# Kernel tuning notes

Hardware: AMD Instinct MI355X
Metric: run time of the kernel (lower is better)

## Reference

```python
import jax, jax.numpy as jnp
import numpy as np
from jax import lax

B = 4096
PRO_VOCAB, PRO_LEN, PRO_K = 25, 1000, 8
LIG_VOCAB, LIG_LEN, LIG_K = 64, 100, 4
CH = 96  # 2*CH = 192 = 6*32 per the reshape in the original forward
DN = ('NCH', 'OIH', 'NCH')  # 1D conv dimension numbers


def setup_inputs() -> dict:
    key = jax.random.key(0)
    ks = jax.random.split(key, 8)
    protein = jax.random.normal(ks[0], (B, PRO_VOCAB, PRO_LEN), dtype=jnp.float32)
    ligand = jax.random.normal(ks[1], (B, LIG_VOCAB, LIG_LEN), dtype=jnp.float32)
    w_pro = jax.random.normal(ks[2], (CH, PRO_VOCAB, PRO_K), dtype=jnp.float32) * 0.05
    b_pro = jnp.zeros((CH,), dtype=jnp.float32)
    w_lig = jax.random.normal(ks[3], (CH, LIG_VOCAB, LIG_K), dtype=jnp.float32) * 0.05
    b_lig = jnp.zeros((CH,), dtype=jnp.float32)
    # QuLinear readout over the 32*32=1024 amplitude-encoded Gram matrix -> scalar
    w_aff = jax.random.normal(ks[4], (1024,), dtype=jnp.float32) * 0.05
    b_aff = jnp.zeros((), dtype=jnp.float32)
    return {"protein": protein, "ligand": ligand, "w_pro": w_pro, "b_pro": b_pro,
            "w_lig": w_lig, "b_lig": b_lig, "w_aff": w_aff, "b_aff": b_aff}


def _conv_branch(x, w, b):
    # Conv1d (valid) -> ReLU -> global max pool over length  =>  (B, CH)
    y = lax.conv_general_dilated(x, w, (1,), 'VALID', dimension_numbers=DN)
    return jnp.max(jax.nn.relu(y + b[None, :, None]), axis=-1)


def reference(protein, ligand, w_pro, b_pro, w_lig, b_lig, w_aff, b_aff):
    x1 = _conv_branch(ligand, w_lig, b_lig)    # (B, 96)
    x2 = _conv_branch(protein, w_pro, b_pro)   # (B, 96)
    x = jnp.concatenate([x1, x2], axis=1).reshape(-1, 6, 32)  # (B, 6, 32)
    # Vectorized per-sample Gram matrix a.T @ a : (B, 32, 32)
    gram = jnp.einsum('bij,bik->bjk', x, x)
    flat = gram.reshape(gram.shape[0], -1)     # (B, 1024)
    # Amplitude encoding: L2-normalize the flattened Gram matrix per sample
    amp = flat / (jnp.linalg.norm(flat, axis=1, keepdims=True) + 1e-12)
    # QuLinear readout -> scalar affinity per sample
    aff = amp @ w_aff + b_aff                  # (B,)
    return aff
```

## Files before the change

### kernel.cpp

```cpp
#include <hip/hip_runtime.h>
#include <math.h>

typedef _Float16 f16;
typedef _Float16 f16x2 __attribute__((ext_vector_type(2)));
typedef _Float16 f16x4 __attribute__((ext_vector_type(4)));
typedef _Float16 f16x8 __attribute__((ext_vector_type(8)));
typedef float f32x4 __attribute__((ext_vector_type(4)));

__global__ void repack_pro_kernel(const float* __restrict__ w, f16* __restrict__ wp) {
    constexpr int V = 25, K = 8;
    int i = blockIdx.x * 256 + threadIdx.x;
    if (i >= K * 6 * 64 * 8) return;
    int e = i & 7, l = (i >> 3) & 63, c6 = (i >> 9) % 6, t = i / (512 * 6);
    int r16 = l & 15, g = l >> 4;
    int ch = c6 * 16 + r16, v = g * 8 + e;
    float val = (v < V) ? w[(ch * V + v) * K + t] : 0.f;
    wp[i] = (f16)val;
}

__global__ void repack_lig_kernel(const float* __restrict__ w, f16* __restrict__ wp) {
    constexpr int V = 64, K = 4;
    int i = blockIdx.x * 256 + threadIdx.x;
    if (i >= 8 * 6 * 64 * 8) return;
    int e = i & 7, l = (i >> 3) & 63, c6 = (i >> 9) % 6, tk = i / (512 * 6);
    int t = tk >> 1, ks = tk & 1;
    int r16 = l & 15, g = l >> 4;
    int ch = c6 * 16 + r16, v = ks * 32 + g * 8 + e;
    wp[i] = (f16)w[(ch * V + v) * K + t];
}

__global__ __launch_bounds__(512, 4) void conv_kernel(
    const float* __restrict__ pro,
    const f16*   __restrict__ wpP,
    const float* __restrict__ bP,
    const float* __restrict__ lig,
    const f16*   __restrict__ wpL,
    const float* __restrict__ bL,
    float* __restrict__ feat,
    int B)
{
    __shared__ __align__(16) char s_raw[264 * 80];
    __shared__ __align__(16) f16  s_w[24576];
    __shared__ float s_red[8 * 96];

    const int tid  = threadIdx.x;
    const int wave = tid >> 6;
    const int lane = tid & 63;
    const int g    = lane >> 4;
    const int r16  = lane & 15;

    if ((int)blockIdx.x < B) {
        constexpr int V = 25, L = 1000, KT = 8, LOUT = 993;
        constexpr int CH = 256, NC = 4, BR = 264, RSB = 80;
        constexpr int P4 = BR / 4;
        constexpr int NU = 7 * P4;
        const size_t b = blockIdx.x;
        const float* gs = pro + b * (size_t)(V * L);
        const int rw = wave & 3, cw = wave >> 2;

        {   const f16x8* wg = (const f16x8*)wpP;
            f16x8* wl = (f16x8*)s_w;
            #pragma unroll
            for (int u = 0; u < 24576 / 8 / 512; ++u)
                wl[u * 512 + tid] = wg[u * 512 + tid];
        }
        for (int row = tid; row < BR; row += 512) {
            const int swz = ((row >> 3) & 3) << 4;
            *(f16x8*)(s_raw + row * RSB + (48 ^ swz)) = (f16x8){};
        }
        __syncthreads();

        float runmax[3];
        #pragma unroll
        for (int c3 = 0; c3 < 3; ++c3) runmax[c3] = -3.0e38f;

        for (int c = 0; c < NC; ++c) {
            if (c) __syncthreads();
            if (tid < NU) {
                const int vq = tid / P4, p4 = tid - vq * P4;
                const int p = 4 * p4, gp = c * CH + p;
                float4 x0 = {0.f,0.f,0.f,0.f}, x1 = {0.f,0.f,0.f,0.f};
                float4 x2 = {0.f,0.f,0.f,0.f}, x3 = {0.f,0.f,0.f,0.f};
                if (gp < L) {
                    x0 = *(const float4*)(gs + (size_t)(4 * vq) * L + gp);
                    if (vq < 6) {
                        x1 = *(const float4*)(gs + (size_t)(4 * vq + 1) * L + gp);
                        x2 = *(const float4*)(gs + (size_t)(4 * vq + 2) * L + gp);
                        x3 = *(const float4*)(gs + (size_t)(4 * vq + 3) * L + gp);
                    }
                }
                const int pb = 8 * vq;
                const int slot = pb & 48, sub = pb & 8;
                const float a0[4] = {x0.x, x0.y, x0.z, x0.w};
                const float a1[4] = {x1.x, x1.y, x1.z, x1.w};
                const float a2[4] = {x2.x, x2.y, x2.z, x2.w};
                const float a3[4] = {x3.x, x3.y, x3.z, x3.w};
                #pragma unroll
                for (int j = 0; j < 4; ++j) {
                    const int row = p + j;
                    const int swz = ((row >> 3) & 3) << 4;
                    f16x4 hv = { (f16)a0[j], (f16)a1[j], (f16)a2[j], (f16)a3[j] };
                    *(f16x4*)(s_raw + row * RSB + ((slot ^ swz) + sub)) = hv;
                }
            }
            __syncthreads();

            f32x4 acc[4][3] = {};
            #pragma unroll 1
            for (int t = 0; t < KT; ++t) {
                f16x8 bf[3];
                #pragma unroll
                for (int c3 = 0; c3 < 3; ++c3)
                    bf[c3] = *(const f16x8*)(s_w + ((t * 6 + cw * 3 + c3) * 64 + lane) * 8);
                #pragma unroll
                for (int rt = 0; rt < 4; ++rt) {
                    const int row = rw * 64 + rt * 16 + r16 + t;
                    const int swz = ((row >> 3) & 3) << 4;
                    f16x8 a = *(const f16x8*)(s_raw + row * RSB + ((g * 16) ^ swz));
                    #pragma unroll
                    for (int c3 = 0; c3 < 3; ++c3)
                        acc[rt][c3] = __builtin_amdgcn_mfma_f32_16x16x32_f16(a, bf[c3], acc[rt][c3], 0, 0, 0);
                }
            }
            #pragma unroll
            for (int rt = 0; rt < 4; ++rt) {
                const int pt = c * CH + rw * 64 + rt * 16;
                if (pt + 16 <= LOUT) {
                    #pragma unroll
                    for (int c3 = 0; c3 < 3; ++c3)
                        #pragma unroll
                        for (int i = 0; i < 4; ++i)
                            runmax[c3] = fmaxf(runmax[c3], acc[rt][c3][i]);
                } else {
                    const int p0g = pt + g * 4;
                    #pragma unroll
                    for (int c3 = 0; c3 < 3; ++c3)
                        #pragma unroll
                        for (int i = 0; i < 4; ++i)
                            if (p0g + i < LOUT) runmax[c3] = fmaxf(runmax[c3], acc[rt][c3][i]);
                }
            }
        }

        #pragma unroll
        for (int c3 = 0; c3 < 3; ++c3) {
            runmax[c3] = fmaxf(runmax[c3], __shfl_xor(runmax[c3], 16, 64));
            runmax[c3] = fmaxf(runmax[c3], __shfl_xor(runmax[c3], 32, 64));
        }
        if (lane < 16) {
            #pragma unroll
            for (int c3 = 0; c3 < 3; ++c3)
                s_red[wave * 48 + c3 * 16 + lane] = runmax[c3];
        }
        __syncthreads();
        if (tid < 96) {
            const int cw2 = tid / 48, chs = tid - cw2 * 48;
            float m = s_red[(cw2 * 4) * 48 + chs];
            #pragma unroll
            for (int rw2 = 1; rw2 < 4; ++rw2)
                m = fmaxf(m, s_red[(cw2 * 4 + rw2) * 48 + chs]);
            feat[b * 192 + 96 + tid] = fmaxf(m + bP[tid], 0.f);
        }
    } else {
        constexpr int V = 64, L = 100, KT = 4, LOUT = 97;
        constexpr int BR = 120, RSB = 144;
        constexpr int P4 = BR / 4, NU = 32 * P4;
        const size_t b = blockIdx.x - B;
        const float* gs = lig + b * (size_t)(V * L);

        {   const f16x8* wg = (const f16x8*)wpL;
            f16x8* wl = (f16x8*)s_w;
            #pragma unroll
            for (int u = 0; u < 24576 / 8 / 512; ++u)
                wl[u * 512 + tid] = wg[u * 512 + tid];
        }
        #pragma unroll
        for (int u = 0; u < 2; ++u) {
            const int i = u * 512 + tid;
            if (i < NU) {
                const int v2 = i / P4, p4 = i - v2 * P4;
                const int p  = 4 * p4;
                float4 x0 = {0.f, 0.f, 0.f, 0.f}, x1 = {0.f, 0.f, 0.f, 0.f};
                if (p < L) {
                    x0 = *(const float4*)(gs + (size_t)(2 * v2) * L + p);
                    x1 = *(const float4*)(gs + (size_t)(2 * v2 + 1) * L + p);
                }
                const int pb = 4 * v2;
                const int slot = pb & 0x70, sub = pb & 12;
                const float vx0[4] = {x0.x, x0.y, x0.z, x0.w};
                const float vx1[4] = {x1.x, x1.y, x1.z, x1.w};
                #pragma unroll
                for (int j = 0; j < 4; ++j) {
                    const int row = p + j;
                    const int swz = ((row >> 3) & 3) << 4;
                    f16x2 hv = { (f16)vx0[j], (f16)vx1[j] };
                    *(f16x2*)(s_raw + row * RSB + ((slot ^ swz) + sub)) = hv;
                }
            }
        }
        __syncthreads();

        if (wave < 7) {
            f32x4 acc[6] = {};
            #pragma unroll 1
            for (int t = 0; t < KT; ++t) {
                #pragma unroll
                for (int ks = 0; ks < 2; ++ks) {
                    f16x8 bf[6];
                    #pragma unroll
                    for (int c6 = 0; c6 < 6; ++c6)
                        bf[c6] = *(const f16x8*)(s_w + (((t * 2 + ks) * 6 + c6) * 64 + lane) * 8);
                    const int row = wave * 16 + r16 + t;
                    const int swz = ((row >> 3) & 3) << 4;
                    f16x8 a = *(const f16x8*)(s_raw + row * RSB + ((ks * 64 + g * 16) ^ swz));
                    #pragma unroll
                    for (int c6 = 0; c6 < 6; ++c6)
                        acc[c6] = __builtin_amdgcn_mfma_f32_16x16x32_f16(a, bf[c6], acc[c6], 0, 0, 0);
                }
            }
            float runmax[6];
            const int p0g = wave * 16 + g * 4;
            #pragma unroll
            for (int c6 = 0; c6 < 6; ++c6) {
                runmax[c6] = -3.0e38f;
                #pragma unroll
                for (int i = 0; i < 4; ++i)
                    if (p0g + i < LOUT) runmax[c6] = fmaxf(runmax[c6], acc[c6][i]);
                runmax[c6] = fmaxf(runmax[c6], __shfl_xor(runmax[c6], 16, 64));
                runmax[c6] = fmaxf(runmax[c6], __shfl_xor(runmax[c6], 32, 64));
            }
            if (lane < 16) {
                #pragma unroll
                for (int c6 = 0; c6 < 6; ++c6)
                    s_red[wave * 96 + c6 * 16 + lane] = runmax[c6];
            }
        }
        __syncthreads();
        if (tid < 96) {
            float m = s_red[tid];
            #pragma unroll
            for (int w = 1; w < 7; ++w) m = fmaxf(m, s_red[w * 96 + tid]);
            feat[b * 192 + tid] = fmaxf(m + bL[tid], 0.f);
        }
    }
}

__global__ __launch_bounds__(256) void gram_affinity_kernel(
    const float* __restrict__ feat, const float* __restrict__ w_aff,
    const float* __restrict__ b_aff, float* __restrict__ out, int B)
{
    const int lane = threadIdx.x & 63;
    const int wid  = threadIdx.x >> 6;
    const int b    = blockIdx.x * 4 + wid;

    __shared__ float s_x[4][192];

    if (b < B) {
        const float* fp = feat + (size_t)b * 192;
        for (int i = lane; i < 192; i += 64) s_x[wid][i] = fp[i];
    }
    __syncthreads();

    if (b < B) {
        float ssum = 0.f, sdot = 0.f;
        #pragma unroll
        for (int t = 0; t < 16; ++t) {
            const int jk = t * 64 + lane;
            const int j = jk >> 5, k = jk & 31;
            float gg = 0.f;
            #pragma unroll
            for (int i = 0; i < 6; ++i)
                gg = fmaf(s_x[wid][i * 32 + j], s_x[wid][i * 32 + k], gg);
            ssum = fmaf(gg, gg, ssum);
            sdot = fmaf(gg, w_aff[jk], sdot);
        }
        #pragma unroll
        for (int off = 32; off >= 1; off >>= 1) {
            ssum += __shfl_xor(ssum, off, 64);
            sdot += __shfl_xor(sdot, off, 64);
        }
        if (lane == 0) out[b] = sdot / (sqrtf(ssum) + 1e-12f) + b_aff[0];
    }
}

extern "C" void kernel_launch(void* const* d_in, const int* in_sizes, int n_in,
                              void* d_out, int out_size, void* d_ws, size_t ws_size,
                              hipStream_t stream)
{
    const float* protein = (const float*)d_in[0];
    const float* ligand  = (const float*)d_in[1];
    const float* w_pro   = (const float*)d_in[2];
    const float* b_pro   = (const float*)d_in[3];
    const float* w_lig   = (const float*)d_in[4];
    const float* b_lig   = (const float*)d_in[5];
    const float* w_aff   = (const float*)d_in[6];
    const float* b_aff   = (const float*)d_in[7];
    float* out = (float*)d_out;
    const int B = out_size;

    float* feat   = (float*)d_ws;
    f16*   wpackP = (f16*)((char*)d_ws + (size_t)B * 192 * 4);
    f16*   wpackL = wpackP + 24576;

    repack_pro_kernel<<<96, 256, 0, stream>>>(w_pro, wpackP);
    repack_lig_kernel<<<96, 256, 0, stream>>>(w_lig, wpackL);

    conv_kernel<<<2 * B, 512, 0, stream>>>(
        protein, wpackP, b_pro, ligand, wpackL, b_lig, feat, B);

    gram_affinity_kernel<<<(B + 3) / 4, 256, 0, stream>>>(feat, w_aff, b_aff, out, B);
}
```

Baseline: 245.2 us.

## Switch conv MFMA to 32x32x16 tiles with 256-thread blocks

Both conv branches move from 16x16x32 MFMA to 32x32x16 MFMA, with the weights repacked into matching 32-channel-by-16-k fragments and the shared-memory input layout adapted. Blocks drop from 512 to 256 threads (4 waves), and each wave now covers 64 output positions across all 96 channels. The larger tiles aim to raise MFMA operand reuse and cut LDS reads per FLOP. The cost is more accumulator registers per wave and fewer waves per block to hide load latency, and the ligand branch now pads its positions to 136.

After: 262.1 us. 6.9% more time.

```diff
diff --git a/kernel.cpp b/kernel.cpp
--- a/kernel.cpp
+++ b/kernel.cpp
@@ -5,15 +5,15 @@
 typedef _Float16 f16x2 __attribute__((ext_vector_type(2)));
 typedef _Float16 f16x4 __attribute__((ext_vector_type(4)));
 typedef _Float16 f16x8 __attribute__((ext_vector_type(8)));
-typedef float f32x4 __attribute__((ext_vector_type(4)));
+typedef float f32x16 __attribute__((ext_vector_type(16)));
 
 __global__ void repack_pro_kernel(const float* __restrict__ w, f16* __restrict__ wp) {
     constexpr int V = 25, K = 8;
     int i = blockIdx.x * 256 + threadIdx.x;
-    if (i >= K * 6 * 64 * 8) return;
-    int e = i & 7, l = (i >> 3) & 63, c6 = (i >> 9) % 6, t = i / (512 * 6);
-    int r16 = l & 15, g = l >> 4;
-    int ch = c6 * 16 + r16, v = g * 8 + e;
+    if (i >= 24576) return;
+    int e = i & 7, l = (i >> 3) & 63, c3 = (i >> 9) % 3, tk = i / (512 * 3);
+    int t = tk >> 1, ks = tk & 1;
+    int ch = c3 * 32 + (l & 31), v = ks * 16 + (l >> 5) * 8 + e;
     float val = (v < V) ? w[(ch * V + v) * K + t] : 0.f;
     wp[i] = (f16)val;
 }
@@ -21,15 +21,14 @@
 __global__ void repack_lig_kernel(const float* __restrict__ w, f16* __restrict__ wp) {
     constexpr int V = 64, K = 4;
     int i = blockIdx.x * 256 + threadIdx.x;
-    if (i >= 8 * 6 * 64 * 8) return;
-    int e = i & 7, l = (i >> 3) & 63, c6 = (i >> 9) % 6, tk = i / (512 * 6);
-    int t = tk >> 1, ks = tk & 1;
-    int r16 = l & 15, g = l >> 4;
-    int ch = c6 * 16 + r16, v = ks * 32 + g * 8 + e;
+    if (i >= 24576) return;
+    int e = i & 7, l = (i >> 3) & 63, c3 = (i >> 9) % 3, tk = i / (512 * 3);
+    int t = tk >> 2, ks = tk & 3;
+    int ch = c3 * 32 + (l & 31), v = ks * 16 + (l >> 5) * 8 + e;
     wp[i] = (f16)w[(ch * V + v) * K + t];
 }
 
-__global__ __launch_bounds__(512, 4) void conv_kernel(
+__global__ __launch_bounds__(256, 2) void conv_kernel(
     const float* __restrict__ pro,
     const f16*   __restrict__ wpP,
     const float* __restrict__ bP,
@@ -41,13 +40,13 @@
 {
     __shared__ __align__(16) char s_raw[264 * 80];
     __shared__ __align__(16) f16  s_w[24576];
-    __shared__ float s_red[8 * 96];
+    __shared__ float s_red[4 * 96];
 
     const int tid  = threadIdx.x;
     const int wave = tid >> 6;
     const int lane = tid & 63;
-    const int g    = lane >> 4;
-    const int r16  = lane & 15;
+    const int q    = lane >> 5;
+    const int r31  = lane & 31;
 
     if ((int)blockIdx.x < B) {
         constexpr int V = 25, L = 1000, KT = 8, LOUT = 993;
@@ -56,15 +55,14 @@
         constexpr int NU = 7 * P4;
         const size_t b = blockIdx.x;
         const float* gs = pro + b * (size_t)(V * L);
-        const int rw = wave & 3, cw = wave >> 2;
 
         {   const f16x8* wg = (const f16x8*)wpP;
             f16x8* wl = (f16x8*)s_w;
             #pragma unroll
-            for (int u = 0; u < 24576 / 8 / 512; ++u)
-                wl[u * 512 + tid] = wg[u * 512 + tid];
-        }
-        for (int row = tid; row < BR; row += 512) {
+            for (int u = 0; u < 12; ++u)
+                wl[u * 256 + tid] = wg[u * 256 + tid];
+        }
+        for (int row = tid; row < BR; row += 256) {
             const int swz = ((row >> 3) & 3) << 4;
             *(f16x8*)(s_raw + row * RSB + (48 ^ swz)) = (f16x8){};
         }
@@ -76,21 +74,124 @@
 
         for (int c = 0; c < NC; ++c) {
             if (c) __syncthreads();
-            if (tid < NU) {
-                const int vq = tid / P4, p4 = tid - vq * P4;
-                const int p = 4 * p4, gp = c * CH + p;
+            #pragma unroll
+            for (int u = 0; u < 2; ++u) {
+                const int i = u * 256 + tid;
+                if (i < NU) {
+                    const int vq = i / P4, p4 = i - vq * P4;
+                    const int p = 4 * p4, gp = c * CH + p;
+                    float4 x0 = {0.f,0.f,0.f,0.f}, x1 = {0.f,0.f,0.f,0.f};
+                    float4 x2 = {0.f,0.f,0.f,0.f}, x3 = {0.f,0.f,0.f,0.f};
+                    if (gp < L) {
+                        x0 = *(const float4*)(gs + (size_t)(4 * vq) * L + gp);
+                        if (vq < 6) {
+                            x1 = *(const float4*)(gs + (size_t)(4 * vq + 1) * L + gp);
+                            x2 = *(const float4*)(gs + (size_t)(4 * vq + 2) * L + gp);
+                            x3 = *(const float4*)(gs + (size_t)(4 * vq + 3) * L + gp);
+                        }
+                    }
+                    const int pb = 8 * vq;
+                    const int slot = pb & 48, sub = pb & 8;
+                    const float a0[4] = {x0.x, x0.y, x0.z, x0.w};
+                    const float a1[4] = {x1.x, x1.y, x1.z, x1.w};
+                    const float a2[4] = {x2.x, x2.y, x2.z, x2.w};
+                    const float a3[4] = {x3.x, x3.y, x3.z, x3.w};
+                    #pragma unroll
+                    for (int j = 0; j < 4; ++j) {
+                        const int row = p + j;
+                        const int swz = ((row >> 3) & 3) << 4;
+                        f16x4 hv = { (f16)a0[j], (f16)a1[j], (f16)a2[j], (f16)a3[j] };
+                        *(f16x4*)(s_raw + row * RSB + ((slot ^ swz) + sub)) = hv;
+                    }
+                }
+            }
+            __syncthreads();
+
+            f32x16 acc[2][3] = {};
+            #pragma unroll 1
+            for (int t = 0; t < KT; ++t) {
+                #pragma unroll
+                for (int ks = 0; ks < 2; ++ks) {
+                    f16x8 bf[3];
+                    #pragma unroll
+                    for (int c3 = 0; c3 < 3; ++c3)
+                        bf[c3] = *(const f16x8*)(s_w + (((t * 2 + ks) * 3 + c3) * 64 + lane) * 8);
+                    #pragma unroll
+                    for (int tt = 0; tt < 2; ++tt) {
+                        const int row = wave * 64 + tt * 32 + r31 + t;
+                        const int swz = ((row >> 3) & 3) << 4;
+                        f16x8 a = *(const f16x8*)(s_raw + row * RSB + (((ks * 32 + q * 16)) ^ swz));
+                        #pragma unroll
+                        for (int c3 = 0; c3 < 3; ++c3)
+                            acc[tt][c3] = __builtin_amdgcn_mfma_f32_32x32x16_f16(a, bf[c3], acc[tt][c3], 0, 0, 0);
+                    }
+                }
+            }
+            #pragma unroll
+            for (int tt = 0; tt < 2; ++tt) {
+                const int pt = c * CH + wave * 64 + tt * 32;
+                if (pt + 32 <= LOUT) {
+                    #pragma unroll
+                    for (int c3 = 0; c3 < 3; ++c3)
+                        #pragma unroll
+                        for (int i = 0; i < 16; ++i)
+                            runmax[c3] = fmaxf(runmax[c3], acc[tt][c3][i]);
+                } else {
+                    #pragma unroll
+                    for (int c3 = 0; c3 < 3; ++c3)
+                        #pragma unroll
+                        for (int i = 0; i < 16; ++i) {
+                            const int rr = (i & 3) + 8 * (i >> 2) + 4 * q;
+                            if (pt + rr < LOUT) runmax[c3] = fmaxf(runmax[c3], acc[tt][c3][i]);
+                        }
+                }
+            }
+        }
+
+        #pragma unroll
+        for (int c3 = 0; c3 < 3; ++c3)
+            runmax[c3] = fmaxf(runmax[c3], __shfl_xor(runmax[c3], 32, 64));
+        if (lane < 32) {
+            #pragma unroll
+            for (int c3 = 0; c3 < 3; ++c3)
+                s_red[wave * 96 + c3 * 32 + r31] = runmax[c3];
+        }
+        __syncthreads();
+        if (tid < 96) {
+            float m = fmaxf(fmaxf(s_red[tid], s_red[96 + tid]),
+                            fmaxf(s_red[192 + tid], s_red[288 + tid]));
+            feat[b * 192 + 96 + tid] = fmaxf(m + bP[tid], 0.f);
+        }
+    } else {
+        constexpr int V = 64, L = 100, KT = 4, LOUT = 97;
+        constexpr int BR = 136, RSB = 144;
+        constexpr int P4 = BR / 4;
+        constexpr int NU = 16 * P4;
+        const size_t b = blockIdx.x - B;
+        const float* gs = lig + b * (size_t)(V * L);
+
+        {   const f16x8* wg = (const f16x8*)wpL;
+            f16x8* wl = (f16x8*)s_w;
+            #pragma unroll
+            for (int u = 0; u < 12; ++u)
+                wl[u * 256 + tid] = wg[u * 256 + tid];
+        }
+        #pragma unroll
+        for (int u = 0; u < 3; ++u) {
+            const int i = u * 256 + tid;
+            if (i < NU) {
+                const int vq = i / P4, p4 = i - vq * P4;
+                const int p = 4 * p4;
                 float4 x0 = {0.f,0.f,0.f,0.f}, x1 = {0.f,0.f,0.f,0.f};
                 float4 x2 = {0.f,0.f,0.f,0.f}, x3 = {0.f,0.f,0.f,0.f};
-                if (gp < L) {
-                    x0 = *(const float4*)(gs + (size_t)(4 * vq) * L + gp);
-                    if (vq < 6) {
-                        x1 = *(const float4*)(gs + (size_t)(4 * vq + 1) * L + gp);
-                        x2 = *(const float4*)(gs + (size_t)(4 * vq + 2) * L + gp);
-                        x3 = *(const float4*)(gs + (size_t)(4 * vq + 3) * L + gp);
-                    }
+                if (p < L) {
+                    x0 = *(const float4*)(gs + (size_t)(4 * vq) * L + p);
+                    x1 = *(const float4*)(gs + (size_t)(4 * vq + 1) * L + p);
+                    x2 = *(const float4*)(gs + (size_t)(4 * vq + 2) * L + p);
+                    x3 = *(const float4*)(gs + (size_t)(4 * vq + 3) * L + p);
                 }
                 const int pb = 8 * vq;
-                const int slot = pb & 48, sub = pb & 8;
+                const int slot = pb & 0x70, sub = pb & 8;
                 const float a0[4] = {x0.x, x0.y, x0.z, x0.w};
                 const float a1[4] = {x1.x, x1.y, x1.z, x1.w};
                 const float a2[4] = {x2.x, x2.y, x2.z, x2.w};
@@ -103,143 +204,46 @@
                     *(f16x4*)(s_raw + row * RSB + ((slot ^ swz) + sub)) = hv;
                 }
             }
-            __syncthreads();
-
-            f32x4 acc[4][3] = {};
-            #pragma unroll 1
-            for (int t = 0; t < KT; ++t) {
+        }
+        __syncthreads();
+
+        f32x16 acc[3] = {};
+        #pragma unroll 1
+        for (int t = 0; t < KT; ++t) {
+            #pragma unroll
+            for (int ks = 0; ks < 4; ++ks) {
                 f16x8 bf[3];
                 #pragma unroll
                 for (int c3 = 0; c3 < 3; ++c3)
-                    bf[c3] = *(const f16x8*)(s_w + ((t * 6 + cw * 3 + c3) * 64 + lane) * 8);
+                    bf[c3] = *(const f16x8*)(s_w + (((t * 4 + ks) * 3 + c3) * 64 + lane) * 8);
+                const int row = wave * 32 + r31 + t;
+                const int swz = ((row >> 3) & 3) << 4;
+                f16x8 a = *(const f16x8*)(s_raw + row * RSB + (((ks * 32 + q * 16)) ^ swz));
                 #pragma unroll
-                for (int rt = 0; rt < 4; ++rt) {
-                    const int row = rw * 64 + rt * 16 + r16 + t;
-                    const int swz = ((row >> 3) & 3) << 4;
-                    f16x8 a = *(const f16x8*)(s_raw + row * RSB + ((g * 16) ^ swz));
-                    #pragma unroll
-                    for (int c3 = 0; c3 < 3; ++c3)
-                        acc[rt][c3] = __builtin_amdgcn_mfma_f32_16x16x32_f16(a, bf[c3], acc[rt][c3], 0, 0, 0);
-                }
-            }
-            #pragma unroll
-            for (int rt = 0; rt < 4; ++rt) {
-                const int pt = c * CH + rw * 64 + rt * 16;
-                if (pt + 16 <= LOUT) {
-                    #pragma unroll
-                    for (int c3 = 0; c3 < 3; ++c3)
-                        #pragma unroll
-                        for (int i = 0; i < 4; ++i)
-                            runmax[c3] = fmaxf(runmax[c3], acc[rt][c3][i]);
-                } else {
-                    const int p0g = pt + g * 4;
-                    #pragma unroll
-                    for (int c3 = 0; c3 < 3; ++c3)
-                        #pragma unroll
-                        for (int i = 0; i < 4; ++i)
-                            if (p0g + i < LOUT) runmax[c3] = fmaxf(runmax[c3], acc[rt][c3][i]);
-                }
-            }
-        }
-
+                for (int c3 = 0; c3 < 3; ++c3)
+                    acc[c3] = __builtin_amdgcn_mfma_f32_32x32x16_f16(a, bf[c3], acc[c3], 0, 0, 0);
+            }
+        }
+        float runmax[3];
         #pragma unroll
         for (int c3 = 0; c3 < 3; ++c3) {
-            runmax[c3] = fmaxf(runmax[c3], __shfl_xor(runmax[c3], 16, 64));
+            runmax[c3] = -3.0e38f;
+            #pragma unroll
+            for (int i = 0; i < 16; ++i) {
+                const int rr = (i & 3) + 8 * (i >> 2) + 4 * q;
+                if (wave * 32 + rr < LOUT) runmax[c3] = fmaxf(runmax[c3], acc[c3][i]);
+            }
             runmax[c3] = fmaxf(runmax[c3], __shfl_xor(runmax[c3], 32, 64));
         }
-        if (lane < 16) {
+        if (lane < 32) {
             #pragma unroll
             for (int c3 = 0; c3 < 3; ++c3)
-                s_red[wave * 48 + c3 * 16 + lane] = runmax[c3];
+                s_red[wave * 96 + c3 * 32 + r31] = runmax[c3];
         }
         __syncthreads();
         if (tid < 96) {
-            const int cw2 = tid / 48, chs = tid - cw2 * 48;
-            float m = s_red[(cw2 * 4) * 48 + chs];
-            #pragma unroll
-            for (int rw2 = 1; rw2 < 4; ++rw2)
-                m = fmaxf(m, s_red[(cw2 * 4 + rw2) * 48 + chs]);
-            feat[b * 192 + 96 + tid] = fmaxf(m + bP[tid], 0.f);
-        }
-    } else {
-        constexpr int V = 64, L = 100, KT = 4, LOUT = 97;
-        constexpr int BR = 120, RSB = 144;
-        constexpr int P4 = BR / 4, NU = 32 * P4;
-        const size_t b = blockIdx.x - B;
-        const float* gs = lig + b * (size_t)(V * L);
-
-        {   const f16x8* wg = (const f16x8*)wpL;
-            f16x8* wl = (f16x8*)s_w;
-            #pragma unroll
-            for (int u = 0; u < 24576 / 8 / 512; ++u)
-                wl[u * 512 + tid] = wg[u * 512 + tid];
-        }
-        #pragma unroll
-        for (int u = 0; u < 2; ++u) {
-            const int i = u * 512 + tid;
-            if (i < NU) {
-                const int v2 = i / P4, p4 = i - v2 * P4;
-                const int p  = 4 * p4;
-                float4 x0 = {0.f, 0.f, 0.f, 0.f}, x1 = {0.f, 0.f, 0.f, 0.f};
-                if (p < L) {
-                    x0 = *(const float4*)(gs + (size_t)(2 * v2) * L + p);
-                    x1 = *(const float4*)(gs + (size_t)(2 * v2 + 1) * L + p);
-                }
-                const int pb = 4 * v2;
-                const int slot = pb & 0x70, sub = pb & 12;
-                const float vx0[4] = {x0.x, x0.y, x0.z, x0.w};
-                const float vx1[4] = {x1.x, x1.y, x1.z, x1.w};
-                #pragma unroll
-                for (int j = 0; j < 4; ++j) {
-                    const int row = p + j;
-                    const int swz = ((row >> 3) & 3) << 4;
-                    f16x2 hv = { (f16)vx0[j], (f16)vx1[j] };
-                    *(f16x2*)(s_raw + row * RSB + ((slot ^ swz) + sub)) = hv;
-                }
-            }
-        }
-        __syncthreads();
-
-        if (wave < 7) {
-            f32x4 acc[6] = {};
-            #pragma unroll 1
-            for (int t = 0; t < KT; ++t) {
-                #pragma unroll
-                for (int ks = 0; ks < 2; ++ks) {
-                    f16x8 bf[6];
-                    #pragma unroll
-                    for (int c6 = 0; c6 < 6; ++c6)
-                        bf[c6] = *(const f16x8*)(s_w + (((t * 2 + ks) * 6 + c6) * 64 + lane) * 8);
-                    const int row = wave * 16 + r16 + t;
-                    const int swz = ((row >> 3) & 3) << 4;
-                    f16x8 a = *(const f16x8*)(s_raw + row * RSB + ((ks * 64 + g * 16) ^ swz));
-                    #pragma unroll
-                    for (int c6 = 0; c6 < 6; ++c6)
-                        acc[c6] = __builtin_amdgcn_mfma_f32_16x16x32_f16(a, bf[c6], acc[c6], 0, 0, 0);
-                }
-            }
-            float runmax[6];
-            const int p0g = wave * 16 + g * 4;
-            #pragma unroll
-            for (int c6 = 0; c6 < 6; ++c6) {
-                runmax[c6] = -3.0e38f;
-                #pragma unroll
-                for (int i = 0; i < 4; ++i)
-                    if (p0g + i < LOUT) runmax[c6] = fmaxf(runmax[c6], acc[c6][i]);
-                runmax[c6] = fmaxf(runmax[c6], __shfl_xor(runmax[c6], 16, 64));
-                runmax[c6] = fmaxf(runmax[c6], __shfl_xor(runmax[c6], 32, 64));
-            }
-            if (lane < 16) {
-                #pragma unroll
-                for (int c6 = 0; c6 < 6; ++c6)
-                    s_red[wave * 96 + c6 * 16 + lane] = runmax[c6];
-            }
-        }
-        __syncthreads();
-        if (tid < 96) {
-            float m = s_red[tid];
-            #pragma unroll
-            for (int w = 1; w < 7; ++w) m = fmaxf(m, s_red[w * 96 + tid]);
+            float m = fmaxf(fmaxf(s_red[tid], s_red[96 + tid]),
+                            fmaxf(s_red[192 + tid], s_red[288 + tid]));
             feat[b * 192 + tid] = fmaxf(m + bL[tid], 0.f);
         }
     }
@@ -305,7 +309,7 @@
     repack_pro_kernel<<<96, 256, 0, stream>>>(w_pro, wpackP);
     repack_lig_kernel<<<96, 256, 0, stream>>>(w_lig, wpackL);
 
-    conv_kernel<<<2 * B, 512, 0, stream>>>(
+    conv_kernel<<<2 * B, 256, 0, stream>>>(
         protein, wpackP, b_pro, ligand, wpackL, b_lig, feat, B);
 
     gram_affinity_kernel<<<(B + 3) / 4, 256, 0, stream>>>(feat, w_aff, b_aff, out, B);
```
